# Kernel optimization log

Measured on AMD Instinct MI355X. Metric: run time of the kernel, lower is better.

The kernel has to match this reference:

```python
import jax, jax.numpy as jnp
import numpy as np

DEMO_T = 4
N_HEADS = 4
N_LAYERS = 2
EPS = 1e-5
IN_DIM = 512
FF_DIM = 128
TEMP = float(np.sqrt(IN_DIM))  # temperature=None -> sqrt(in_dim)


def setup_inputs() -> dict:
    key = jax.random.key(0)
    ks = jax.random.split(key, 12)
    B, d, T, H, W = 8, IN_DIM, 36, 7, 12
    s_in = 1.0 / np.sqrt(d)
    s_ff = 1.0 / np.sqrt(FF_DIM)
    f32 = jnp.float32
    return {
        "inputs": jax.random.normal(ks[0], (B, d, T, H, W), f32),
        "demo_wq": jax.random.normal(ks[1], (N_LAYERS, FF_DIM, d), f32) * s_in,
        "demo_wk": jax.random.normal(ks[2], (N_LAYERS, FF_DIM, d), f32) * s_in,
        "demo_wv": jax.random.normal(ks[3], (N_LAYERS, FF_DIM, d), f32) * s_in,
        "demo_wo": jax.random.normal(ks[4], (N_LAYERS, d, FF_DIM), f32) * s_ff,
        "obs_wq": jax.random.normal(ks[5], (N_LAYERS, FF_DIM, d), f32) * s_in,
        "obs_wk": jax.random.normal(ks[6], (N_LAYERS, FF_DIM, d), f32) * s_in,
        "obs_wv": jax.random.normal(ks[7], (N_LAYERS, FF_DIM, d), f32) * s_in,
        "obs_wo": jax.random.normal(ks[8], (N_LAYERS, d, FF_DIM), f32) * s_ff,
        "bn_gamma": jnp.ones((N_LAYERS, d), f32),
        "bn_beta": jnp.zeros((N_LAYERS, d), f32),
    }


def _conv1x1(w, x):
    # 1x1x1 Conv3d, bias=False == per-voxel channel mixing
    return jnp.einsum('od,bdthw->bothw', w, x)


def _forward(inputs, demo_wq, demo_wk, demo_wv, demo_wo,
             obs_wq, obs_wk, obs_wv, obs_wo, bn_gamma, bn_beta):
    B, d, T, H, W = inputs.shape
    HW = H * W
    obs_T = T - DEMO_T
    neg_inf = jnp.asarray(-jnp.inf, inputs.dtype)
    # causal log-mask over demo tokens, block-expanded to spatial positions
    tril = jnp.tril(jnp.ones((DEMO_T, DEMO_T), inputs.dtype))
    mask = jnp.repeat(jnp.repeat(tril, HW, axis=0), HW, axis=1)  # (dTHW, dTHW)
    log_mask = jnp.where(mask > 0, jnp.asarray(0.0, inputs.dtype), neg_inf)

    x = inputs
    for i in range(N_LAYERS):
        demo_in = x[:, :, :DEMO_T]   # [B,d,dT,H,W]
        obs_in = x[:, :, DEMO_T:]    # [B,d,oT,H,W]

        # --- demo self-attention (causal) ---
        def demo_heads(w):
            y = _conv1x1(w, demo_in)                      # [B,ff,dT,H,W]
            return y.reshape(B, N_HEADS, -1, DEMO_T * HW)  # [B,n,ch,dTHW]
        dq, dk, dv = demo_heads(demo_wq[i]), demo_heads(demo_wk[i]), demo_heads(demo_wv[i])
        dkq = jnp.einsum('bnci,bncj->bnij', dk, dq) / TEMP + log_mask
        dattn = jax.nn.softmax(dkq, axis=-1)               # softmax over j (as in source)
        dv_att = jnp.einsum('bncj,bnij->bnci', dv, dattn)  # attended demo values
        # NOTE: the source computes demo_out via demo_Outs + relu-skip but never
        # uses it downstream (dead code); only dv_att/dk feed the obs fusion.

        # --- obs attention, fused with demo keys/attended-values ---
        def obs_heads(w):
            y = _conv1x1(w, obs_in)                        # [B,ff,oT,H,W]
            y = y.reshape(B, N_HEADS, -1, obs_T, HW)
            return jnp.transpose(y, (0, 3, 1, 2, 4))       # [B,oT,n,ch,HW]
        oq, ok, ov = obs_heads(obs_wq[i]), obs_heads(obs_wk[i]), obs_heads(obs_wv[i])
        rep_k = jnp.broadcast_to(dk[:, None], (B, obs_T) + dk.shape[1:])
        rep_v = jnp.broadcast_to(dv_att[:, None], (B, obs_T) + dv_att.shape[1:])
        cat_k = jnp.concatenate([rep_k, ok], axis=-1)      # [B,oT,n,ch,(1+dT)HW]
        cat_v = jnp.concatenate([rep_v, ov], axis=-1)
        okq = jnp.einsum('btnci,btncj->btnij', cat_k, oq) / TEMP  # i=cat len, j=HW
        oattn = jax.nn.softmax(okq, axis=-1)               # softmax over j (source: dim=4)
        ov_att = jnp.einsum('btncj,btnji->btnci', cat_v, oattn)  # [B,oT,n,ch,HW]
        obs_out = _conv1x1(obs_wo[i],
                           jnp.transpose(ov_att, (0, 2, 3, 1, 4)).reshape(B, -1, obs_T, H, W))
        # skip (out_dim == in_dim), dropout=0 -> identity
        obs_res = obs_in + jax.nn.relu(obs_out)

        # shared BatchNorm3d (training-mode batch stats) over concatenated streams
        x = jnp.concatenate([demo_in, obs_res], axis=2)
        mean = x.mean(axis=(0, 2, 3, 4)).reshape(1, -1, 1, 1, 1)
        var = x.var(axis=(0, 2, 3, 4)).reshape(1, -1, 1, 1, 1)
        g = bn_gamma[i].reshape(1, -1, 1, 1, 1)
        b = bn_beta[i].reshape(1, -1, 1, 1, 1)
        x = g * (x - mean) * jax.lax.rsqrt(var + EPS) + b
    return x  # == out_dict['last']


def reference(inputs, demo_wq, demo_wk, demo_wv, demo_wo,
              obs_wq, obs_wk, obs_wv, obs_wo, bn_gamma, bn_beta):
    return _forward(inputs, demo_wq, demo_wk, demo_wv, demo_wo,
                    obs_wq, obs_wk, obs_wv, obs_wo, bn_gamma, bn_beta)
```

## Files before the change

### kernel.cpp

```cpp
#include <hip/hip_runtime.h>

#define B_N 8
#define D_N 512
#define T_N 36
#define HW_N 84
#define THW_N 3024
#define DT_N 4
#define OT_N 32
#define NH_N 4
#define FF_N 128
#define CH_N 32
#define DI_N 336
#define OI_N 2688
#define CAT_N 420
#define INV_TEMP 0.04419417382415922f
#define BN_EPS 1e-5f
#define INV_CNT (1.0f / 24192.0f)

#define SW_DWQ 0
#define SW_DWK 131072
#define SW_DWV 262144
#define SW_OWQ 393216
#define SW_OWK 524288
#define SW_OWV 655360
#define SW_OWO 786432
#define S_DQ   917504
#define S_DK   1261568
#define S_DV   1605632
#define S_DVA  1949696
#define S_OQ   2293760
#define S_OK   5046272
#define S_OV   7798784
#define S_OVA  10551296
#define S_XBF  13303808

typedef short bf16x8 __attribute__((ext_vector_type(8)));
typedef float f32x4 __attribute__((ext_vector_type(4)));
typedef unsigned int u32;

#define GLD16(SRC, DST) __builtin_amdgcn_global_load_lds( \
    (const __attribute__((address_space(1))) u32*)(SRC), \
    (__attribute__((address_space(3))) u32*)(DST), 16, 0, 0)

__device__ __forceinline__ short f2bf(float f) {
    unsigned u = __float_as_uint(f);
    u += 0x7fffu + ((u >> 16) & 1u);
    return (short)(u >> 16);
}
__device__ __forceinline__ float bf2f(short s) {
    return __uint_as_float(((unsigned)(unsigned short)s) << 16);
}

__global__ __launch_bounds__(256) void cvt_w_kernel(
    const float* __restrict__ s0, const float* __restrict__ s1,
    const float* __restrict__ s2, const float* __restrict__ s3,
    const float* __restrict__ s4, const float* __restrict__ s5,
    const float* __restrict__ s6, short* __restrict__ dst,
    float* __restrict__ stats)
{
    const int bid = blockIdx.x;
    if (bid == 0) {
        #pragma unroll
        for (int k = 0; k < 8; ++k) stats[threadIdx.x * 8 + k] = 0.f;
    }
    const int a = bid >> 6, blk = bid & 63;
    const float* src;
    switch (a) {
        case 0: src = s0; break; case 1: src = s1; break;
        case 2: src = s2; break; case 3: src = s3; break;
        case 4: src = s4; break; case 5: src = s5; break;
        default: src = s6;
    }
    const int idx = (blk * 256 + (int)threadIdx.x) * 8;
    float4 f0 = *reinterpret_cast<const float4*>(src + idx);
    float4 f1 = *reinterpret_cast<const float4*>(src + idx + 4);
    bf16x8 pk;
    pk[0] = f2bf(f0.x); pk[1] = f2bf(f0.y); pk[2] = f2bf(f0.z); pk[3] = f2bf(f0.w);
    pk[4] = f2bf(f1.x); pk[5] = f2bf(f1.y); pk[6] = f2bf(f1.z); pk[7] = f2bf(f1.w);
    size_t dstoff;
    if (a < 6) {
        const int layer = idx >> 16;
        const int w = idx & 65535;
        const int mg = w >> 9;
        const int k  = w & 511;
        const int p  = k >> 6;
        const int kc = (k >> 3) & 7;
        const int mh = mg >> 6;
        const int m  = mg & 63;
        dstoff = (size_t)layer * 65536 +
                 (size_t)(((p * 2 + mh) * 8 + kc) * 64 + m) * 8;
    } else {
        dstoff = idx;
    }
    *reinterpret_cast<bf16x8*>(dst + (size_t)a * 131072 + dstoff) = pk;
}

__global__ __launch_bounds__(256) void xin_kernel(
    const float* __restrict__ in_f, short* __restrict__ xbf,
    float* __restrict__ stats0)
{
    __shared__ short tile[48][65];
    __shared__ float red_s[16][64];
    __shared__ float red_q[16][64];

    const int bid = blockIdx.x;
    const int b = bid / 504, rem = bid % 504, tt = rem >> 3, cblk = rem & 7;
    const int t0 = tt * 48, c0 = cblk * 64;
    const int tid = threadIdx.x;
    const bool is_demo = (tt < 7);

    #pragma unroll
    for (int l0 = 0; l0 < 768; l0 += 256) {
        int l = l0 + tid;
        int cc = l / 12, tg = l % 12;
        size_t addr = ((size_t)b * D_N + c0 + cc) * THW_N + t0 + tg * 4;
        float4 v = *reinterpret_cast<const float4*>(in_f + addr);
        tile[tg * 4 + 0][cc] = f2bf(v.x);
        tile[tg * 4 + 1][cc] = f2bf(v.y);
        tile[tg * 4 + 2][cc] = f2bf(v.z);
        tile[tg * 4 + 3][cc] = f2bf(v.w);
    }
    __syncthreads();
    float psum[4] = {}, psq[4] = {};
    const int cg = tid & 15;
    #pragma unroll
    for (int l0 = 0; l0 < 768; l0 += 256) {
        int l = l0 + tid;
        int tk = l >> 4;
        short4 s4;
        s4.x = tile[tk][cg * 4 + 0];
        s4.y = tile[tk][cg * 4 + 1];
        s4.z = tile[tk][cg * 4 + 2];
        s4.w = tile[tk][cg * 4 + 3];
        *reinterpret_cast<short4*>(
            xbf + ((size_t)b * THW_N + t0 + tk) * 512 + c0 + cg * 4) = s4;
        if (is_demo) {
            float v0 = bf2f(s4.x), v1 = bf2f(s4.y), v2 = bf2f(s4.z), v3 = bf2f(s4.w);
            psum[0] += v0; psum[1] += v1; psum[2] += v2; psum[3] += v3;
            psq[0] += v0 * v0; psq[1] += v1 * v1; psq[2] += v2 * v2; psq[3] += v3 * v3;
        }
    }
    if (!is_demo) return;
    __syncthreads();
    #pragma unroll
    for (int j = 0; j < 4; ++j) {
        red_s[tid >> 4][cg * 4 + j] = psum[j];
        red_q[tid >> 4][cg * 4 + j] = psq[j];
    }
    __syncthreads();
    if (tid < 64) {
        float s = 0.f, q = 0.f;
        #pragma unroll
        for (int r = 0; r < 16; ++r) { s += red_s[r][tid]; q += red_q[r][tid]; }
        atomicAdd(&stats0[c0 + tid], s);
        atomicAdd(&stats0[512 + c0 + tid], q);
    }
}

__global__ __launch_bounds__(256) void proj_mfma_kernel(
    const short* __restrict__ xbf, short* __restrict__ ws, int layer)
{
    __shared__ short As[3][4096];
    __shared__ short Bs[3072];

    const int tid = threadIdx.x;
    const int lane = tid & 63, wv = tid >> 6;
    const int l15 = lane & 15, q = lane >> 4;

    const int bid = blockIdx.x;
    const int mh = bid & 1;
    const int rem = bid >> 1;
    const int b = rem / 63, ct = rem - b * 63;
    const bool is_demo = (ct < 7);
    const int woff = layer * 65536;
    const short* W0 = ws + (is_demo ? SW_DWQ : SW_OWQ) + woff;
    const short* W1 = ws + (is_demo ? SW_DWK : SW_OWK) + woff;
    const short* W2 = ws + (is_demo ? SW_DWV : SW_OWV) + woff;
    const int Ltok = is_demo ? DI_N : OI_N;
    const int colL = is_demo ? ct * 48 : (ct - 7) * 48;
    short* Yq = ws + (is_demo ? S_DQ : S_OQ);
    short* Yk = ws + (is_demo ? S_DK : S_OK);
    short* Yv = ws + (is_demo ? S_DV : S_OV);
    const short* Xb = xbf + ((size_t)b * THW_N + (is_demo ? 0 : DI_N) + colL) * 512;

    const short* rp[3];
    rp[0] = W0 + (size_t)mh * 4096 + lane * 8;
    rp[1] = W1 + (size_t)mh * 4096 + lane * 8;
    rp[2] = W2 + (size_t)mh * 4096 + lane * 8;
    const short* bp[2];
    #pragma unroll
    for (int h = 0; h < 2; ++h) {
        int c = h * 192 + wv * 64 + lane;
        bp[h] = Xb + (size_t)(c % 48) * 512 + (c / 48) * 8;
    }

    f32x4 acc[3][3] = {};

    for (int k0 = 0; k0 < D_N; k0 += 64) {
        const size_t poff = (size_t)(k0 >> 6) * 8192;
        __syncthreads();
        #pragma unroll
        for (int h = 0; h < 2; ++h) {
            #pragma unroll
            for (int wt = 0; wt < 3; ++wt)
                GLD16(rp[wt] + poff + (h * 256 + wv * 64) * 8,
                      &As[wt][(h * 256 + wv * 64) * 8]);
        }
        if (wv < 3) {
            GLD16(bp[0] + k0, &Bs[(wv * 64) * 8]);
            GLD16(bp[1] + k0, &Bs[(192 + wv * 64) * 8]);
        }
        __syncthreads();

        #pragma unroll
        for (int kk = 0; kk < 2; ++kk) {
            const int kc = kk * 4 + q;
            bf16x8 bfr[3];
            #pragma unroll
            for (int nt = 0; nt < 3; ++nt)
                bfr[nt] = *reinterpret_cast<const bf16x8*>(
                    &Bs[(kc * 48 + nt * 16 + l15) * 8]);
            #pragma unroll
            for (int wt = 0; wt < 3; ++wt) {
                bf16x8 afr = *reinterpret_cast<const bf16x8*>(
                    &As[wt][(kc * 64 + wv * 16 + l15) * 8]);
                #pragma unroll
                for (int nt = 0; nt < 3; ++nt)
                    acc[wt][nt] = __builtin_amdgcn_mfma_f32_16x16x32_bf16(
                        afr, bfr[nt], acc[wt][nt], 0, 0, 0);
            }
        }
    }

    const int mrow = mh * 64 + wv * 16 + q * 4;
    #pragma unroll
    for (int nt = 0; nt < 3; ++nt) {
        const int token = colL + nt * 16 + l15;
        f32x4 aq = acc[0][nt] * INV_TEMP;
        short4 s4;
        s4.x = f2bf(aq[0]); s4.y = f2bf(aq[1]); s4.z = f2bf(aq[2]); s4.w = f2bf(aq[3]);
        *reinterpret_cast<short4*>(Yq + ((size_t)b * Ltok + token) * 128 + mrow) = s4;
        f32x4 ak = acc[1][nt];
        s4.x = f2bf(ak[0]); s4.y = f2bf(ak[1]); s4.z = f2bf(ak[2]); s4.w = f2bf(ak[3]);
        *reinterpret_cast<short4*>(Yk + ((size_t)b * Ltok + token) * 128 + mrow) = s4;
        #pragma unroll
        for (int rr = 0; rr < 4; ++rr)
            Yv[((size_t)b * FF_N + mrow + rr) * Ltok + token] = f2bf(acc[2][nt][rr]);
    }
}

template<int NT>
__device__ __forceinline__ void demo_core(
    const short* __restrict__ dqS, const short* __restrict__ dkS,
    const short* __restrict__ dvS, short* __restrict__ dvaS,
    short* __restrict__ Pt, int b, int n, int ti, int ih)
{
    constexpr int NTP = (NT + 1) & ~1;
    const int tid = threadIdx.x;
    const int lane = tid & 63, w = tid >> 6;
    const int l15 = lane & 15, q = lane >> 4;
    const int jmax = (ti + 1) * 84;

    const int irow = ih * 48 + w * 16 + l15;
    const int tokA = ti * 84 + (irow < 84 ? irow : 83);
    bf16x8 afr = *reinterpret_cast<const bf16x8*>(
        dkS + ((size_t)b * DI_N + tokA) * 128 + n * 32 + q * 8);

    f32x4 s[NT];
    #pragma unroll
    for (int nt = 0; nt < NT; ++nt) {
        bf16x8 bfr = *reinterpret_cast<const bf16x8*>(
            dqS + ((size_t)b * DI_N + nt * 16 + l15) * 128 + n * 32 + q * 8);
        f32x4 z = {};
        s[nt] = __builtin_amdgcn_mfma_f32_16x16x32_bf16(afr, bfr, z, 0, 0, 0);
    }

    const int mstart = jmax - (NT - 1) * 16;
    #pragma unroll
    for (int r = 0; r < 4; ++r) {
        if (l15 >= mstart) s[NT - 1][r] = -3.0e38f;
        float mx = s[0][r];
        #pragma unroll
        for (int nt = 1; nt < NT; ++nt) mx = fmaxf(mx, s[nt][r]);
        #pragma unroll
        for (int o = 1; o < 16; o <<= 1) mx = fmaxf(mx, __shfl_xor(mx, o));
        float sm = 0.f;
        #pragma unroll
        for (int nt = 0; nt < NT; ++nt) {
            float e = __expf(s[nt][r] - mx);
            s[nt][r] = e; sm += e;
        }
        #pragma unroll
        for (int o = 1; o < 16; o <<= 1) sm += __shfl_xor(sm, o);
        float inv = 1.f / sm;
        #pragma unroll
        for (int nt = 0; nt < NT; ++nt) s[nt][r] *= inv;
    }

    #pragma unroll
    for (int nt = 0; nt < NT; ++nt)
        #pragma unroll
        for (int r = 0; r < 4; ++r)
            Pt[(w * 16 + q * 4 + r) * 360 + nt * 16 + l15] = f2bf(s[nt][r]);
    if (NTP != NT) {
        #pragma unroll
        for (int r = 0; r < 4; ++r)
            Pt[(w * 16 + q * 4 + r) * 360 + NT * 16 + l15] = 0;
    }
    __syncthreads();

    f32x4 oacc[2] = {};
    #pragma unroll
    for (int kk = 0; kk < NTP / 2; ++kk) {
        bf16x8 pb = *reinterpret_cast<const bf16x8*>(
            &Pt[(w * 16 + l15) * 360 + kk * 32 + q * 8]);
        #pragma unroll
        for (int ct = 0; ct < 2; ++ct) {
            bf16x8 va = *reinterpret_cast<const bf16x8*>(
                dvS + ((size_t)b * FF_N + n * 32 + ct * 16 + l15) * DI_N + kk * 32 + q * 8);
            oacc[ct] = __builtin_amdgcn_mfma_f32_16x16x32_bf16(va, pb, oacc[ct], 0, 0, 0);
        }
    }

    const int ig = ih * 48 + w * 16 + l15;
    if (ig < 84) {
        #pragma unroll
        for (int ct = 0; ct < 2; ++ct)
            #pragma unroll
            for (int r = 0; r < 4; ++r)
                dvaS[((size_t)b * FF_N + n * 32 + ct * 16 + q * 4 + r) * DI_N + ti * 84 + ig] =
                    f2bf(oacc[ct][r]);
    }
}

__global__ __launch_bounds__(192) void demo_attn_mfma_kernel(const short* __restrict__ ws)
{
    __shared__ short Pt[48 * 360];

    const short* dqS = ws + S_DQ;
    const short* dkS = ws + S_DK;
    const short* dvS = ws + S_DV;
    short* dvaS = const_cast<short*>(ws) + S_DVA;

    const int bid = blockIdx.x;
    const int ih = bid & 1, ti = (bid >> 1) & 3;
    const int n = (bid >> 3) & 3, b = bid >> 5;

    switch (ti) {
        case 0: demo_core<6>(dqS, dkS, dvS, dvaS, Pt, b, n, ti, ih); break;
        case 1: demo_core<11>(dqS, dkS, dvS, dvaS, Pt, b, n, ti, ih); break;
        case 2: demo_core<16>(dqS, dkS, dvS, dvaS, Pt, b, n, ti, ih); break;
        default: demo_core<21>(dqS, dkS, dvS, dvaS, Pt, b, n, ti, ih); break;
    }
}

__global__ __launch_bounds__(256, 4) void obs_attn_mfma_kernel(const short* __restrict__ ws)
{
    __shared__ short Pt[2][96 * 72];

    const short* dkS = ws + S_DK;
    const short* dvaS = ws + S_DVA;
    const short* oqS = ws + S_OQ;
    const short* okS = ws + S_OK;
    const short* ovS = ws + S_OV;
    short* ovaS = const_cast<short*>(ws) + S_OVA;

    const int bid = blockIdx.x;
    const int b = bid >> 7, rem = bid & 127, t = rem >> 2, n = rem & 3;

    const int tid = threadIdx.x;
    const int lane = tid & 63, wv = tid >> 6;
    const int l15 = lane & 15, q = lane >> 4;

    bf16x8 bfr[6];
    #pragma unroll
    for (int nt = 0; nt < 6; ++nt) {
        int j = nt * 16 + l15; if (j > 83) j = 83;
        bfr[nt] = *reinterpret_cast<const bf16x8*>(
            oqS + ((size_t)b * OI_N + t * 84 + j) * 128 + n * 32 + q * 8);
    }

    const int pv_mt = wv & 1;
    const int pv_nb = wv >> 1;
    const int cg = n * 32 + pv_mt * 16 + l15;
    const short* dvaRow = dvaS + ((size_t)b * FF_N + cg) * DI_N;
    const short* ovRow  = ovS + ((size_t)b * FF_N + cg) * OI_N + t * 84;

    f32x4 oacc[3] = {};

    #pragma unroll
    for (int it = 0; it < 7; ++it) {
        const int jc = it * 64;

        int jg = jc + wv * 16 + l15; if (jg > 419) jg = 419;
        bf16x8 afr = (jg < DI_N)
            ? *reinterpret_cast<const bf16x8*>(
                  dkS + ((size_t)b * DI_N + jg) * 128 + n * 32 + q * 8)
            : *reinterpret_cast<const bf16x8*>(
                  okS + ((size_t)b * OI_N + t * 84 + jg - DI_N) * 128 + n * 32 + q * 8);

        f32x4 s[6];
        #pragma unroll
        for (int nt = 0; nt < 6; ++nt) {
            f32x4 z = {};
            s[nt] = __builtin_amdgcn_mfma_f32_16x16x32_bf16(afr, bfr[nt], z, 0, 0, 0);
        }
        float inv[4];
        #pragma unroll
        for (int r = 0; r < 4; ++r) {
            if (l15 >= 4) s[5][r] = -3.0e38f;
            float m2 = s[0][r];
            #pragma unroll
            for (int nt2 = 1; nt2 < 6; ++nt2) m2 = fmaxf(m2, s[nt2][r]);
            #pragma unroll
            for (int o = 1; o < 16; o <<= 1) m2 = fmaxf(m2, __shfl_xor(m2, o));
            float sm = 0.f;
            #pragma unroll
            for (int nt2 = 0; nt2 < 6; ++nt2) { float e = __expf(s[nt2][r] - m2); s[nt2][r] = e; sm += e; }
            #pragma unroll
            for (int o = 1; o < 16; o <<= 1) sm += __shfl_xor(sm, o);
            inv[r] = 1.f / sm;
        }
        short* Pw = &Pt[it & 1][0];
        const int ibase = jc + wv * 16 + q * 4;
        #pragma unroll
        for (int nt = 0; nt < 6; ++nt) {
            short4 pk4;
            pk4.x = (ibase + 0 < CAT_N) ? f2bf(s[nt][0] * inv[0]) : (short)0;
            pk4.y = (ibase + 1 < CAT_N) ? f2bf(s[nt][1] * inv[1]) : (short)0;
            pk4.z = (ibase + 2 < CAT_N) ? f2bf(s[nt][2] * inv[2]) : (short)0;
            pk4.w = (ibase + 3 < CAT_N) ? f2bf(s[nt][3] * inv[3]) : (short)0;
            *reinterpret_cast<short4*>(&Pw[(nt * 16 + l15) * 72 + wv * 16 + q * 4]) = pk4;
        }
        __syncthreads();

        #pragma unroll
        for (int kk = 0; kk < 2; ++kk) {
            const int i0 = jc + kk * 32 + q * 8;
            bf16x8 va = (i0 < DI_N)
                ? *reinterpret_cast<const bf16x8*>(dvaRow + i0)
                : *reinterpret_cast<const bf16x8*>(ovRow + (i0 - DI_N));
            #pragma unroll
            for (int u = 0; u < 3; ++u) {
                int nt = pv_nb + u * 2;
                bf16x8 pb = *reinterpret_cast<const bf16x8*>(
                    &Pw[(nt * 16 + l15) * 72 + kk * 32 + q * 8]);
                oacc[u] = __builtin_amdgcn_mfma_f32_16x16x32_bf16(va, pb, oacc[u], 0, 0, 0);
            }
        }
    }

    #pragma unroll
    for (int u = 0; u < 3; ++u) {
        int i = (pv_nb + u * 2) * 16 + l15;
        if (i < HW_N) {
            short4 st;
            st.x = f2bf(oacc[u][0]); st.y = f2bf(oacc[u][1]);
            st.z = f2bf(oacc[u][2]); st.w = f2bf(oacc[u][3]);
            *reinterpret_cast<short4*>(
                ovaS + (((size_t)b * OT_N + t) * 84 + i) * 128 + n * 32 + pv_mt * 16 + q * 4) = st;
        }
    }
}

__global__ __launch_bounds__(256) void outproj_mfma_kernel(
    short* __restrict__ xbf, const short* __restrict__ ws, int layer,
    float* __restrict__ stats)
{
    __shared__ float redS[4][32];
    __shared__ float redQ[4][32];

    const int bid = blockIdx.x;
    const int t8 = bid & 7;
    const int rr = bid >> 3;
    const int c32 = rr & 15;
    const int tc = rr >> 4;
    const int tchunk = tc * 8 + t8;
    const int o0 = c32 * 32;

    const int tid = threadIdx.x;
    const int lane = tid & 63, wv = tid >> 6;
    const int l15 = lane & 15, q = lane >> 4;

    const int g0 = tchunk * 192 + wv * 48;
    const int b = g0 / OI_N;
    const size_t xbase = (size_t)(g0 + DI_N * (b + 1)) * 512 + o0;

    const short* Wo = ws + SW_OWO + layer * 65536;
    const short* ova = ws + S_OVA;

    short* xp[3][2];
    short4 oldx[3][2];
    #pragma unroll
    for (int nt = 0; nt < 3; ++nt)
        #pragma unroll
        for (int mt = 0; mt < 2; ++mt) {
            xp[nt][mt] = xbf + xbase + (size_t)(nt * 16 + l15) * 512 + mt * 16 + q * 4;
            oldx[nt][mt] = *reinterpret_cast<short4*>(xp[nt][mt]);
        }

    bf16x8 afr[2][4];
    #pragma unroll
    for (int mt = 0; mt < 2; ++mt)
        #pragma unroll
        for (int kc = 0; kc < 4; ++kc)
            afr[mt][kc] = *reinterpret_cast<const bf16x8*>(
                Wo + (size_t)(o0 + mt * 16 + l15) * FF_N + kc * 32 + q * 8);

    float csum[2][4] = {}, csq[2][4] = {};

    #pragma unroll
    for (int nt = 0; nt < 3; ++nt) {
        const int g = g0 + nt * 16;
        const short* ovaT = ova + (size_t)(g + l15) * FF_N + q * 8;
        bf16x8 bfr[4];
        #pragma unroll
        for (int kc = 0; kc < 4; ++kc)
            bfr[kc] = *reinterpret_cast<const bf16x8*>(ovaT + kc * 32);

        f32x4 acc[2] = {};
        #pragma unroll
        for (int kc = 0; kc < 4; ++kc) {
            acc[0] = __builtin_amdgcn_mfma_f32_16x16x32_bf16(afr[0][kc], bfr[kc], acc[0], 0, 0, 0);
            acc[1] = __builtin_amdgcn_mfma_f32_16x16x32_bf16(afr[1][kc], bfr[kc], acc[1], 0, 0, 0);
        }

        #pragma unroll
        for (int mt = 0; mt < 2; ++mt) {
            short4 old4 = oldx[nt][mt];
            float ov[4] = {bf2f(old4.x), bf2f(old4.y), bf2f(old4.z), bf2f(old4.w)};
            short4 nw;
            short* nwp = &nw.x;
            #pragma unroll
            for (int r = 0; r < 4; ++r) {
                float v = acc[mt][r];
                float y = ov[r] + (v > 0.f ? v : 0.f);
                short ybf = f2bf(y);
                nwp[r] = ybf;
                float yr = bf2f(ybf);
                csum[mt][r] += yr;
                csq[mt][r] += yr * yr;
            }
            *reinterpret_cast<short4*>(xp[nt][mt]) = nw;
        }
    }

    #pragma unroll
    for (int mt = 0; mt < 2; ++mt) {
        #pragma unroll
        for (int r = 0; r < 4; ++r) {
            float s = csum[mt][r], qq = csq[mt][r];
            #pragma unroll
            for (int o = 1; o < 16; o <<= 1) {
                s += __shfl_xor(s, o);
                qq += __shfl_xor(qq, o);
            }
            if (l15 == 0) {
                redS[wv][mt * 16 + q * 4 + r] = s;
                redQ[wv][mt * 16 + q * 4 + r] = qq;
            }
        }
    }
    __syncthreads();
    if (tid < 32) {
        float s = redS[0][tid] + redS[1][tid] + redS[2][tid] + redS[3][tid];
        float qq = redQ[0][tid] + redQ[1][tid] + redQ[2][tid] + redQ[3][tid];
        atomicAdd(&stats[o0 + tid], s);
        atomicAdd(&stats[512 + o0 + tid], qq);
    }
}

__global__ __launch_bounds__(256) void bn_mid_kernel(
    short* __restrict__ xbf, const float* __restrict__ stats,
    const float* __restrict__ gamma, const float* __restrict__ beta,
    float* __restrict__ stats_next)
{
    __shared__ float red_s[4][512];
    __shared__ float red_q[4][512];

    const int bid = blockIdx.x;
    const int b = bid / 63, tt = bid % 63;
    const int t0 = tt * 48;
    const bool is_demo = (tt < 7);
    const int tid = threadIdx.x;
    const int chg = tid & 63;
    const int trow = tid >> 6;

    float mean[8], rs[8], g[8], bb[8];
    #pragma unroll
    for (int j = 0; j < 8; ++j) {
        int c = chg * 8 + j;
        float m = stats[c] * INV_CNT;
        float var = stats[512 + c] * INV_CNT - m * m;
        mean[j] = m;
        rs[j] = rsqrtf(var + BN_EPS);
        g[j] = gamma[c];
        bb[j] = beta[c];
    }

    float psum[8] = {}, psq[8] = {};
    #pragma unroll
    for (int it = 0; it < 12; ++it) {
        int tok = t0 + it * 4 + trow;
        short* p = xbf + ((size_t)b * THW_N + tok) * 512 + chg * 8;
        bf16x8 v = *reinterpret_cast<bf16x8*>(p);
        bf16x8 w;
        #pragma unroll
        for (int j = 0; j < 8; ++j) {
            float y = g[j] * (bf2f(v[j]) - mean[j]) * rs[j] + bb[j];
            short yb = f2bf(y);
            w[j] = yb;
            if (is_demo) {
                float yr = bf2f(yb);
                psum[j] += yr; psq[j] += yr * yr;
            }
        }
        *reinterpret_cast<bf16x8*>(p) = w;
    }
    if (!is_demo) return;
    #pragma unroll
    for (int j = 0; j < 8; ++j) {
        red_s[trow][chg * 8 + j] = psum[j];
        red_q[trow][chg * 8 + j] = psq[j];
    }
    __syncthreads();
    #pragma unroll
    for (int h = 0; h < 2; ++h) {
        int c = tid + h * 256;
        float s = red_s[0][c] + red_s[1][c] + red_s[2][c] + red_s[3][c];
        float qq = red_q[0][c] + red_q[1][c] + red_q[2][c] + red_q[3][c];
        atomicAdd(&stats_next[c], s);
        atomicAdd(&stats_next[512 + c], qq);
    }
}

__global__ __launch_bounds__(256) void bn_out_kernel(
    const short* __restrict__ xbf, float* __restrict__ out_f,
    const float* __restrict__ stats,
    const float* __restrict__ gamma, const float* __restrict__ beta)
{
    __shared__ float tile[48][65];

    const int bid = blockIdx.x;
    const int b = bid / 504, rem = bid % 504, tt = rem >> 3, cblk = rem & 7;
    const int t0 = tt * 48, c0 = cblk * 64;
    const int tid = threadIdx.x;
    const int cg = tid & 15;

    float mean[4], rs[4], g[4], bb[4];
    #pragma unroll
    for (int j = 0; j < 4; ++j) {
        int c = c0 + cg * 4 + j;
        float m = stats[c] * INV_CNT;
        float var = stats[512 + c] * INV_CNT - m * m;
        mean[j] = m; rs[j] = rsqrtf(var + BN_EPS);
        g[j] = gamma[c]; bb[j] = beta[c];
    }

    #pragma unroll
    for (int l0 = 0; l0 < 768; l0 += 256) {
        int l = l0 + tid;
        int tok = l >> 4;
        short4 v = *reinterpret_cast<const short4*>(
            xbf + ((size_t)b * THW_N + t0 + tok) * 512 + c0 + cg * 4);
        tile[tok][cg * 4 + 0] = g[0] * (bf2f(v.x) - mean[0]) * rs[0] + bb[0];
        tile[tok][cg * 4 + 1] = g[1] * (bf2f(v.y) - mean[1]) * rs[1] + bb[1];
        tile[tok][cg * 4 + 2] = g[2] * (bf2f(v.z) - mean[2]) * rs[2] + bb[2];
        tile[tok][cg * 4 + 3] = g[3] * (bf2f(v.w) - mean[3]) * rs[3] + bb[3];
    }
    __syncthreads();
    #pragma unroll
    for (int l0 = 0; l0 < 768; l0 += 256) {
        int l = l0 + tid;
        int cc = l / 12, tg = l % 12;
        float4 o;
        o.x = tile[tg * 4 + 0][cc];
        o.y = tile[tg * 4 + 1][cc];
        o.z = tile[tg * 4 + 2][cc];
        o.w = tile[tg * 4 + 3][cc];
        *reinterpret_cast<float4*>(
            out_f + ((size_t)b * D_N + c0 + cc) * THW_N + t0 + tg * 4) = o;
    }
}

extern "C" void kernel_launch(void* const* d_in, const int* in_sizes, int n_in,
                              void* d_out, int out_size, void* d_ws, size_t ws_size,
                              hipStream_t stream)
{
    const float* inp  = (const float*)d_in[0];
    const float* dwq  = (const float*)d_in[1];
    const float* dwk  = (const float*)d_in[2];
    const float* dwv  = (const float*)d_in[3];
    const float* owq  = (const float*)d_in[5];
    const float* owk  = (const float*)d_in[6];
    const float* owv  = (const float*)d_in[7];
    const float* owo  = (const float*)d_in[8];
    const float* gam  = (const float*)d_in[9];
    const float* bet  = (const float*)d_in[10];
    float* x  = (float*)d_out;
    float* stats = (float*)d_ws;
    short* wsS = (short*)(stats + 2048);
    short* xbf = wsS + S_XBF;

    cvt_w_kernel<<<448, 256, 0, stream>>>(dwq, dwk, dwv, owq, owk, owv, owo, wsS, stats);
    xin_kernel<<<4032, 256, 0, stream>>>(inp, xbf, stats);

    for (int layer = 0; layer < 2; ++layer) {
        float* stL = stats + layer * 1024;
        size_t coff = (size_t)layer * D_N;
        proj_mfma_kernel<<<1008, 256, 0, stream>>>(xbf, wsS, layer);
        demo_attn_mfma_kernel<<<256, 192, 0, stream>>>(wsS);
        obs_attn_mfma_kernel<<<1024, 256, 0, stream>>>(wsS);
        outproj_mfma_kernel<<<1792, 256, 0, stream>>>(xbf, wsS, layer, stL);
        if (layer == 0) {
            bn_mid_kernel<<<504, 256, 0, stream>>>(
                xbf, stL, gam + coff, bet + coff, stats + 1024);
        } else {
            bn_out_kernel<<<4032, 256, 0, stream>>>(
                xbf, x, stL, gam + coff, bet + coff);
        }
    }
    (void)in_sizes; (void)n_in; (void)out_size; (void)ws_size;
}
```

Baseline: 306.7 us.

## Double-buffer LDS tiles in projection GEMM with explicit vmcnt waits

Turns the single-buffered K loop of the QKV projection MFMA kernel into a two-stage pipeline. Global-to-LDS loads for stage s+2 are issued while stage s is computed, and explicit s_waitcnt vmcnt counts let each wave wait only on the older stage's loads. This is meant to hide global load latency behind MFMA work. It doubles the LDS footprint to about 60KB per block, which may reduce occupancy, and it relies on hand-counted outstanding loads being correct.

```diff
diff --git a/kernel.cpp b/kernel.cpp
--- a/kernel.cpp
+++ b/kernel.cpp
@@ -160,8 +160,8 @@
 __global__ __launch_bounds__(256) void proj_mfma_kernel(
     const short* __restrict__ xbf, short* __restrict__ ws, int layer)
 {
-    __shared__ short As[3][4096];
-    __shared__ short Bs[3072];
+    __shared__ short As[2][3][4096];
+    __shared__ short Bs[2][3072];
 
     const int tid = threadIdx.x;
     const int lane = tid & 63, wv = tid >> 6;
@@ -196,22 +196,36 @@
 
     f32x4 acc[3][3] = {};
 
-    for (int k0 = 0; k0 < D_N; k0 += 64) {
-        const size_t poff = (size_t)(k0 >> 6) * 8192;
-        __syncthreads();
+    auto ISSUE = [&](int s, int buf) {
+        const size_t poff = (size_t)s * 8192;
         #pragma unroll
         for (int h = 0; h < 2; ++h) {
             #pragma unroll
             for (int wt = 0; wt < 3; ++wt)
                 GLD16(rp[wt] + poff + (h * 256 + wv * 64) * 8,
-                      &As[wt][(h * 256 + wv * 64) * 8]);
+                      &As[buf][wt][(h * 256 + wv * 64) * 8]);
         }
         if (wv < 3) {
-            GLD16(bp[0] + k0, &Bs[(wv * 64) * 8]);
-            GLD16(bp[1] + k0, &Bs[(192 + wv * 64) * 8]);
-        }
-        __syncthreads();
-
+            GLD16(bp[0] + s * 64, &Bs[buf][(wv * 64) * 8]);
+            GLD16(bp[1] + s * 64, &Bs[buf][(192 + wv * 64) * 8]);
+        }
+    };
+
+    ISSUE(0, 0);
+    ISSUE(1, 1);
+
+    #pragma unroll
+    for (int s = 0; s < 8; ++s) {
+        if (s < 7) {
+            if (wv < 3) asm volatile("s_waitcnt vmcnt(8)" ::: "memory");
+            else        asm volatile("s_waitcnt vmcnt(6)" ::: "memory");
+        } else {
+            asm volatile("s_waitcnt vmcnt(0)" ::: "memory");
+        }
+        __builtin_amdgcn_s_barrier();
+        asm volatile("" ::: "memory");
+
+        const int buf = s & 1;
         #pragma unroll
         for (int kk = 0; kk < 2; ++kk) {
             const int kc = kk * 4 + q;
@@ -219,17 +233,22 @@
             #pragma unroll
             for (int nt = 0; nt < 3; ++nt)
                 bfr[nt] = *reinterpret_cast<const bf16x8*>(
-                    &Bs[(kc * 48 + nt * 16 + l15) * 8]);
+                    &Bs[buf][(kc * 48 + nt * 16 + l15) * 8]);
             #pragma unroll
             for (int wt = 0; wt < 3; ++wt) {
                 bf16x8 afr = *reinterpret_cast<const bf16x8*>(
-                    &As[wt][(kc * 64 + wv * 16 + l15) * 8]);
+                    &As[buf][wt][(kc * 64 + wv * 16 + l15) * 8]);
                 #pragma unroll
                 for (int nt = 0; nt < 3; ++nt)
                     acc[wt][nt] = __builtin_amdgcn_mfma_f32_16x16x32_bf16(
                         afr, bfr[nt], acc[wt][nt], 0, 0, 0);
             }
         }
+
+        asm volatile("" ::: "memory");
+        __builtin_amdgcn_s_barrier();
+        asm volatile("" ::: "memory");
+        if (s + 2 < 8) ISSUE(s + 2, buf);
     }
 
     const int mrow = mh * 64 + wv * 16 + q * 4;
```

New measurement: 306.8 us, median of 2. No clear change (+0.0%).
